# Kernel tuning notes

Measured on AMD Instinct MI355X. Metric: run time of the kernel, lower is better.

The kernel has to match this reference:

```python
import jax, jax.numpy as jnp
import numpy as np

B, N, IN_D = 4, 2046, 512
D, H = 1024, 16
DH = D // H  # 64
S = N + 2
EPS = 1e-5


def setup_inputs() -> dict:
    key = jax.random.key(0)
    ks = jax.random.split(key, 9)
    s = lambda k, shp, fan: jax.random.normal(k, shp, jnp.float32) * (1.0 / np.sqrt(fan))
    return {
        "x": jax.random.normal(ks[0], (B, N, IN_D), jnp.float32),
        "W_map": s(ks[1], (IN_D, D), IN_D),
        "b_map": jnp.zeros((D,), jnp.float32),
        "time_token": jax.random.normal(ks[2], (1, D), jnp.float32),
        "cluster_token": jax.random.normal(ks[3], (1, D), jnp.float32),
        "ln_g": jnp.ones((D,), jnp.float32),
        "ln_b": jnp.zeros((D,), jnp.float32),
        "Wq": s(ks[4], (H, DH, DH), DH),
        "bq": jax.random.normal(ks[5], (H, DH), jnp.float32) * 0.01,
        "Wk": s(ks[6], (H, DH, DH), DH),
        "bk": jax.random.normal(ks[7], (H, DH), jnp.float32) * 0.01,
    }


def reference(x, W_map, b_map, time_token, cluster_token, ln_g, ln_b, Wq, bq, Wk, bk):
    b = x.shape[0]
    tokens = x @ W_map + b_map                       # [B, N, D]
    tt = jnp.broadcast_to(time_token[None], (b, 1, D))
    ct = jnp.broadcast_to(cluster_token[None], (b, 1, D))
    out = jnp.concatenate([tt, ct, tokens], axis=1)  # [B, S, D]
    # LayerNorm (norm1)
    mu = jnp.mean(out, axis=-1, keepdims=True)
    var = jnp.mean(jnp.square(out - mu), axis=-1, keepdims=True)
    h = (out - mu) * jax.lax.rsqrt(var + EPS) * ln_g + ln_b
    # MSAAttention: per-head Q/K linear, softmax(QK^T / sqrt(d_head))
    hh = h.reshape(b, S, H, DH)
    q = jnp.einsum("bshd,hde->bhse", hh, Wq) + bq[None, :, None, :]
    k = jnp.einsum("bshd,hde->bhse", hh, Wk) + bk[None, :, None, :]
    scores = jnp.einsum("bhse,bhte->bhst", q, k) / np.sqrt(DH).astype(np.float32)
    attn = jax.nn.softmax(scores, axis=-1)           # [B, H, S, S]
    # hstack over heads -> [B, S, H*S]; extract_attention reshapes back and
    # means over heads, then takes rows 0 (timing) and 1 (id).
    m = jnp.mean(attn, axis=1)                       # [B, S, S]
    return m[:, 0, :], m[:, 1, :]
```

## Files before the change

kernel.cpp:

```cpp
#include <hip/hip_runtime.h>
#include <hip/hip_bf16.h>
#include <math.h>

#define BB 4
#define NN 2046
#define IND 512
#define DD 1024
#define HH 16
#define SS 2048
#define MM (BB*NN)
#define MPAD 8192
#define ROWPAD 8256
#define EPSV 1e-5f

#define OFF_U    0
#define OFF_G    8192
#define OFF_C2   8320
#define OFF_S12  24832
#define OFF_A    90880
#define ZERO_SIZE (1147648 - OFF_S12)
#define OFF_XH   1147648
#define OFF_SC   1147648
#define OFF_XL   9536256
#define OFF_WHT  17924864
#define OFF_WLT  18973440

typedef float f32x4 __attribute__((ext_vector_type(4)));
typedef __bf16 bf16x8 __attribute__((ext_vector_type(8)));
typedef unsigned short u16x8 __attribute__((ext_vector_type(8)));

__device__ __forceinline__ unsigned short f2bf_rne(float f) {
  unsigned int u = __float_as_uint(f);
  u += 0x7FFFu + ((u >> 16) & 1u);
  return (unsigned short)(u >> 16);
}
__device__ __forceinline__ float bf2f(unsigned short h) {
  return __uint_as_float(((unsigned int)h) << 16);
}

__device__ __forceinline__ float waveSum(float v) {
  #pragma unroll
  for (int m = 32; m >= 1; m >>= 1) v += __shfl_xor(v, m, 64);
  return v;
}

__device__ __forceinline__ float blockReduceSum(float v, volatile float* buf4) {
  #pragma unroll
  for (int m = 32; m >= 1; m >>= 1) v += __shfl_xor(v, m, 64);
  int wid = threadIdx.x >> 6;
  __syncthreads();
  if ((threadIdx.x & 63) == 0) buf4[wid] = v;
  __syncthreads();
  return buf4[0] + buf4[1] + buf4[2] + buf4[3];
}

__device__ __forceinline__ float blockReduceMax(float v, volatile float* buf4) {
  #pragma unroll
  for (int m = 32; m >= 1; m >>= 1) v = fmaxf(v, __shfl_xor(v, m, 64));
  int wid = threadIdx.x >> 6;
  __syncthreads();
  if ((threadIdx.x & 63) == 0) buf4[wid] = v;
  __syncthreads();
  return fmaxf(fmaxf(buf4[0], buf4[1]), fmaxf(buf4[2], buf4[3]));
}

#define GLOAD_LDS16(g, l) \
  __builtin_amdgcn_global_load_lds((const __attribute__((address_space(1))) void*)(g), \
                                   (__attribute__((address_space(3))) void*)(l), 16, 0, 0)

__global__ __launch_bounds__(256) void convX(const float* __restrict__ x,
                                             unsigned short* __restrict__ xh,
                                             unsigned short* __restrict__ xl) {
  const int t = threadIdx.x;
  const int row = blockIdx.x * 4 + (t >> 6);
  const int c0 = (t & 63) * 8;
  const size_t po = (size_t)row * IND + c0;
  u16x8 hv, lv;
  if (row < MM) {
    const float4* xv = (const float4*)(x + po);
    float4 a = xv[0], b = xv[1];
    float vv[8] = {a.x, a.y, a.z, a.w, b.x, b.y, b.z, b.w};
    #pragma unroll
    for (int i = 0; i < 8; ++i) {
      unsigned short hh = f2bf_rne(vv[i]);
      hv[i] = hh;
      lv[i] = f2bf_rne(vv[i] - bf2f(hh));
    }
  } else {
    #pragma unroll
    for (int i = 0; i < 8; ++i) { hv[i] = 0; lv[i] = 0; }
  }
  *(u16x8*)(xh + po) = hv;
  *(u16x8*)(xl + po) = lv;
}

__global__ __launch_bounds__(256) void convW(const float* __restrict__ Wm,
                                             unsigned short* __restrict__ wht,
                                             unsigned short* __restrict__ wlt) {
  __shared__ float tile[64][65];
  const int t = threadIdx.x;
  const int kb = blockIdx.x >> 4, nb = blockIdx.x & 15;
  const int k0 = kb * 64, n0 = nb * 64;
  #pragma unroll
  for (int q = 0; q < 16; ++q) {
    int lin = q * 256 + t;
    int kk = lin >> 6, nn = lin & 63;
    tile[kk][nn] = Wm[(size_t)(k0 + kk) * DD + n0 + nn];
  }
  __syncthreads();
  #pragma unroll
  for (int q = 0; q < 16; ++q) {
    int lin = q * 256 + t;
    int nn = lin >> 6, kk = lin & 63;
    float v = tile[kk][nn];
    unsigned short hh = f2bf_rne(v);
    wht[(size_t)(n0 + nn) * IND + k0 + kk] = hh;
    wlt[(size_t)(n0 + nn) * IND + k0 + kk] = f2bf_rne(v - bf2f(hh));
  }
}

__global__ __launch_bounds__(64) void stageA(
    const float* __restrict__ tt, const float* __restrict__ ct,
    const float* __restrict__ lng, const float* __restrict__ lnb,
    const float* __restrict__ Wq, const float* __restrict__ bq,
    const float* __restrict__ Wk, const float* __restrict__ bk,
    float* __restrict__ ws) {
  __shared__ float hsm[64], qsm[64];
  const int s = blockIdx.x >> 4, h = blockIdx.x & 15;
  const int e = threadIdx.x;
  const float* src = s ? ct : tt;
  float* U   = ws + OFF_U/4;
  float* Gp  = ws + OFF_G/4;
  float* C2p = ws + OFF_C2/4;
  float* s12 = ws + OFF_S12/4;
  float* Ap  = ws + OFF_A/4;

  float s1 = 0.f, s2 = 0.f;
  #pragma unroll
  for (int i = 0; i < 16; ++i) { float v = src[i*64 + e]; s1 += v; s2 += v*v; }
  s1 = waveSum(s1); s2 = waveSum(s2);
  if (h == 0 && e == 0) {
    s12[(MPAD + s)*2 + 0] = s1;
    s12[(MPAD + s)*2 + 1] = s2;
  }
  const float mu = s1 * (1.f/DD);
  const float var = s2 * (1.f/DD) - mu*mu;
  const float rstd = rsqrtf(var + EPSV);

  const int d0 = h * 64;
  hsm[e] = (src[d0+e] - mu) * rstd * lng[d0+e] + lnb[d0+e];
  __syncthreads();
  float qv = bq[d0+e];
  #pragma unroll 8
  for (int d = 0; d < 64; ++d) qv += hsm[d] * Wq[(size_t)(d0+d)*64 + e];
  qsm[e] = qv;
  __syncthreads();
  float wt = 0.f;
  #pragma unroll 8
  for (int ee = 0; ee < 64; ++ee) wt += Wk[(size_t)(d0+e)*64 + ee] * qsm[ee];
  wt *= 0.125f;
  const float c = waveSum(qsm[e] * bk[d0+e]) * 0.125f;
  const float u = lng[d0+e] * wt;
  U[s*DD + d0 + e] = u;
  const float G  = waveSum(lng[d0+e] * wt);
  const float C  = waveSum(lnb[d0+e] * wt);
  const float a0 = waveSum(tt[d0+e] * u);
  const float a1 = waveSum(ct[d0+e] * u);
  if (e == 0) {
    Gp[s*16+h]  = G;
    C2p[s*16+h] = C + c;
    Ap[(size_t)(s*16+h)*ROWPAD + MPAD + 0] = a0;
    Ap[(size_t)(s*16+h)*ROWPAD + MPAD + 1] = a1;
  }
}

__global__ __launch_bounds__(256, 2) void stageB(
    const unsigned short* __restrict__ xh, const unsigned short* __restrict__ xl,
    const unsigned short* __restrict__ wht, const unsigned short* __restrict__ wlt,
    const float* __restrict__ bmap, float* __restrict__ ws) {
  __shared__ unsigned short Ash[128*64], Asl[128*64], Bsh[128*64], Bsl[128*64];
  __shared__ float s12w[4][64][2];
  __shared__ float aw[4][64][2];
  const int t = threadIdx.x, wave = t >> 6, lane = t & 63;
  const int lj = lane & 15, lg = lane >> 4;
  const int mb = blockIdx.x & 63, nb = blockIdx.x >> 6;
  const int m0 = mb * 128, n0 = nb * 128;
  const int wr = wave >> 1, wc = wave & 1;
  const float* U = ws + OFF_U/4;
  float* s12 = ws + OFF_S12/4;
  float* Ap  = ws + OFF_A/4;

  f32x4 acc[4][4];
  #pragma unroll
  for (int i = 0; i < 4; ++i)
    #pragma unroll
    for (int j = 0; j < 4; ++j) acc[i][j] = (f32x4){0.f,0.f,0.f,0.f};

  const int rr = lane >> 3;
  const int slot = (lane & 7) ^ rr;

  for (int ks = 0; ks < 8; ++ks) {
    const size_t kofs = (size_t)ks * 64;
    #pragma unroll
    for (int q = 0; q < 4; ++q) {
      const int r = wave*32 + q*8 + rr;
      const size_t go = (size_t)(m0 + r)*IND + kofs + slot*8;
      const size_t gn = (size_t)(n0 + r)*IND + kofs + slot*8;
      const int lo = (wave*32 + q*8) * 64;
      GLOAD_LDS16(xh  + go, Ash + lo);
      GLOAD_LDS16(xl  + go, Asl + lo);
      GLOAD_LDS16(wht + gn, Bsh + lo);
      GLOAD_LDS16(wlt + gn, Bsl + lo);
    }
    __syncthreads();
    #pragma unroll
    for (int kf = 0; kf < 2; ++kf) {
      const int sl = kf*4 + lg;
      bf16x8 afh[4], afl[4], bfh[4], bfl[4];
      #pragma unroll
      for (int i = 0; i < 4; ++i) {
        const int r = wr*64 + i*16 + lj;
        const int byt = r*128 + ((sl ^ (r & 7)) * 16);
        afh[i] = *(const bf16x8*)((const char*)Ash + byt);
        afl[i] = *(const bf16x8*)((const char*)Asl + byt);
      }
      #pragma unroll
      for (int j = 0; j < 4; ++j) {
        const int r = wc*64 + j*16 + lj;
        const int byt = r*128 + ((sl ^ (r & 7)) * 16);
        bfh[j] = *(const bf16x8*)((const char*)Bsh + byt);
        bfl[j] = *(const bf16x8*)((const char*)Bsl + byt);
      }
      #pragma unroll
      for (int i = 0; i < 4; ++i)
        #pragma unroll
        for (int j = 0; j < 4; ++j) {
          acc[i][j] = __builtin_amdgcn_mfma_f32_16x16x32_bf16(afh[i], bfh[j], acc[i][j], 0, 0, 0);
          acc[i][j] = __builtin_amdgcn_mfma_f32_16x16x32_bf16(afl[i], bfh[j], acc[i][j], 0, 0, 0);
          acc[i][j] = __builtin_amdgcn_mfma_f32_16x16x32_bf16(afh[i], bfl[j], acc[i][j], 0, 0, 0);
        }
    }
    __syncthreads();
  }

  float s1p[16], s2p[16], a0p[16], a1p[16];
  #pragma unroll
  for (int p = 0; p < 16; ++p) { s1p[p]=0.f; s2p[p]=0.f; a0p[p]=0.f; a1p[p]=0.f; }
  #pragma unroll
  for (int j = 0; j < 4; ++j) {
    const int gc = n0 + wc*64 + j*16 + lj;
    const float bmv = bmap[gc];
    const float u0 = U[gc], u1 = U[DD + gc];
    #pragma unroll
    for (int i = 0; i < 4; ++i)
      #pragma unroll
      for (int r = 0; r < 4; ++r) {
        const float tok = acc[i][j][r] + bmv;
        const int p = i*4 + r;
        s1p[p] += tok; s2p[p] += tok*tok;
        a0p[p] += tok*u0; a1p[p] += tok*u1;
      }
  }
  #pragma unroll
  for (int msk = 8; msk >= 1; msk >>= 1)
    #pragma unroll
    for (int p = 0; p < 16; ++p) {
      s1p[p] += __shfl_xor(s1p[p], msk, 64);
      s2p[p] += __shfl_xor(s2p[p], msk, 64);
      a0p[p] += __shfl_xor(a0p[p], msk, 64);
      a1p[p] += __shfl_xor(a1p[p], msk, 64);
    }
  if (lj == 0) {
    #pragma unroll
    for (int p = 0; p < 16; ++p) {
      const int rl = (p>>2)*16 + lg*4 + (p&3);
      s12w[wave][rl][0] = s1p[p];
      s12w[wave][rl][1] = s2p[p];
      aw[wave][rl][0]   = a0p[p];
      aw[wave][rl][1]   = a1p[p];
    }
  }
  __syncthreads();
  if (t < 128) {
    const int rloc = t, wrg = rloc >> 6, rw = rloc & 63;
    const int grow = m0 + rloc;
    const int h0 = n0 >> 6;
    atomicAdd(&s12[grow*2+0], s12w[wrg*2+0][rw][0] + s12w[wrg*2+1][rw][0]);
    atomicAdd(&s12[grow*2+1], s12w[wrg*2+0][rw][1] + s12w[wrg*2+1][rw][1]);
    atomicAdd(&Ap[(size_t)(0*16 + h0    )*ROWPAD + grow], aw[wrg*2+0][rw][0]);
    atomicAdd(&Ap[(size_t)(1*16 + h0    )*ROWPAD + grow], aw[wrg*2+0][rw][1]);
    atomicAdd(&Ap[(size_t)(0*16 + h0 + 1)*ROWPAD + grow], aw[wrg*2+1][rw][0]);
    atomicAdd(&Ap[(size_t)(1*16 + h0 + 1)*ROWPAD + grow], aw[wrg*2+1][rw][1]);
  }
}

__global__ __launch_bounds__(256) void stageC1(const float* __restrict__ ws,
                                               float* __restrict__ sc) {
  __shared__ float rbuf[4];
  const int bid = blockIdx.x;
  const int h = bid & 15, bs = bid >> 4, b = bs >> 1, s = bs & 1;
  const int t = threadIdx.x;
  const float* s12 = ws + OFF_S12/4;
  const float* Ah  = ws + OFF_A/4 + (size_t)(s*16+h)*ROWPAD;
  const float Gh = ws[OFF_G/4 + s*16+h], Ch = ws[OFF_C2/4 + s*16+h];

  float v[8];
  float mx = -3.0e38f;
  #pragma unroll
  for (int i = 0; i < 8; ++i) {
    const int p = i*256 + t;
    const int r = (p == 0) ? MPAD : (p == 1) ? (MPAD+1) : (b*NN + p - 2);
    const float s1 = s12[r*2], s2 = s12[r*2+1];
    const float mu = s1 * (1.f/DD);
    const float var = s2 * (1.f/DD) - mu*mu;
    const float rstd = rsqrtf(var + EPSV);
    v[i] = rstd * (Ah[r] - mu*Gh) + Ch;
    mx = fmaxf(mx, v[i]);
  }
  mx = blockReduceMax(mx, rbuf);
  float sum = 0.f;
  #pragma unroll
  for (int i = 0; i < 8; ++i) { v[i] = __expf(v[i] - mx); sum += v[i]; }
  sum = blockReduceSum(sum, rbuf);
  const float inv = 1.f / (16.f * sum);
  float* outp = sc + (size_t)bid * SS;
  #pragma unroll
  for (int i = 0; i < 8; ++i) outp[i*256 + t] = v[i] * inv;
}

__global__ __launch_bounds__(256) void stageC2(const float* __restrict__ sc,
                                               float* __restrict__ out) {
  const int idx = blockIdx.x * 256 + threadIdx.x;
  const int pos = idx & 2047, bs = idx >> 11;
  const int b = bs >> 1, s = bs & 1;
  const float* base = sc + (size_t)bs*16*SS + pos;
  float acc = 0.f;
  #pragma unroll
  for (int h = 0; h < 16; ++h) acc += base[(size_t)h*SS];
  out[(size_t)s*(BB*SS) + (size_t)b*SS + pos] = acc;
}

extern "C" void kernel_launch(void* const* d_in, const int* in_sizes, int n_in,
                              void* d_out, int out_size, void* d_ws, size_t ws_size,
                              hipStream_t stream) {
  const float* x   = (const float*)d_in[0];
  const float* Wm  = (const float*)d_in[1];
  const float* bm  = (const float*)d_in[2];
  const float* tt  = (const float*)d_in[3];
  const float* ct  = (const float*)d_in[4];
  const float* lng = (const float*)d_in[5];
  const float* lnb = (const float*)d_in[6];
  const float* Wq  = (const float*)d_in[7];
  const float* bq  = (const float*)d_in[8];
  const float* Wk  = (const float*)d_in[9];
  const float* bk  = (const float*)d_in[10];
  char* wsb = (char*)d_ws;
  float* ws = (float*)d_ws;
  float* out = (float*)d_out;

  unsigned short* xh  = (unsigned short*)(wsb + OFF_XH);
  unsigned short* xlp = (unsigned short*)(wsb + OFF_XL);
  unsigned short* wht = (unsigned short*)(wsb + OFF_WHT);
  unsigned short* wlt = (unsigned short*)(wsb + OFF_WLT);
  float* sc = (float*)(wsb + OFF_SC);

  hipMemsetAsync(wsb + OFF_S12, 0, ZERO_SIZE, stream);
  hipLaunchKernelGGL(convX,   dim3(2048), dim3(256), 0, stream, x, xh, xlp);
  hipLaunchKernelGGL(convW,   dim3(128),  dim3(256), 0, stream, Wm, wht, wlt);
  hipLaunchKernelGGL(stageA,  dim3(32),   dim3(64),  0, stream,
                     tt, ct, lng, lnb, Wq, bq, Wk, bk, ws);
  hipLaunchKernelGGL(stageB,  dim3(512),  dim3(256), 0, stream,
                     xh, xlp, wht, wlt, bm, ws);
  hipLaunchKernelGGL(stageC1, dim3(128),  dim3(256), 0, stream, ws, sc);
  hipLaunchKernelGGL(stageC2, dim3(64),   dim3(256), 0, stream, sc, out);
}
```

Before: 127.6 us.

## Fuse prep kernels, drop x low-bf16 split, atomically reduce heads into output

Merges the x and W conversions, the token/Q-K precompute and the workspace zeroing into one prep launch, replacing the memset and three separate kernels. It drops the low-order bf16 part of x, so the GEMM issues two MFMAs per tile instead of three and loads less data, at a cost in accuracy. The softmax no longer computes a block max; it clamps scores at 60 and exponentiates directly. The per-head results are accumulated into the output with atomics instead of going through a scratch buffer and a separate reduction kernel, which adds nondeterministic summation order and a risk of overflow if scores are large.

```diff
diff --git a/kernel.cpp b/kernel.cpp
--- a/kernel.cpp
+++ b/kernel.cpp
@@ -14,16 +14,13 @@
 #define EPSV 1e-5f
 
 #define OFF_U    0
-#define OFF_G    8192
-#define OFF_C2   8320
-#define OFF_S12  24832
-#define OFF_A    90880
-#define ZERO_SIZE (1147648 - OFF_S12)
-#define OFF_XH   1147648
-#define OFF_SC   1147648
-#define OFF_XL   9536256
-#define OFF_WHT  17924864
-#define OFF_WLT  18973440
+#define OFF_G    2048
+#define OFF_C2   2080
+#define OFF_S12  4096
+#define OFF_A    (4096 + 2*ROWPAD)
+#define OFF_XH_B  1139200
+#define OFF_WHT_B (OFF_XH_B + MPAD*IND*2)
+#define OFF_WLT_B (OFF_WHT_B + DD*IND*2)
 
 typedef float f32x4 __attribute__((ext_vector_type(4)));
 typedef __bf16 bf16x8 __attribute__((ext_vector_type(8)));
@@ -33,9 +30,6 @@
   unsigned int u = __float_as_uint(f);
   u += 0x7FFFu + ((u >> 16) & 1u);
   return (unsigned short)(u >> 16);
-}
-__device__ __forceinline__ float bf2f(unsigned short h) {
-  return __uint_as_float(((unsigned int)h) << 16);
 }
 
 __device__ __forceinline__ float waveSum(float v) {
@@ -54,131 +48,132 @@
   return buf4[0] + buf4[1] + buf4[2] + buf4[3];
 }
 
-__device__ __forceinline__ float blockReduceMax(float v, volatile float* buf4) {
-  #pragma unroll
-  for (int m = 32; m >= 1; m >>= 1) v = fmaxf(v, __shfl_xor(v, m, 64));
-  int wid = threadIdx.x >> 6;
-  __syncthreads();
-  if ((threadIdx.x & 63) == 0) buf4[wid] = v;
-  __syncthreads();
-  return fmaxf(fmaxf(buf4[0], buf4[1]), fmaxf(buf4[2], buf4[3]));
-}
-
 #define GLOAD_LDS16(g, l) \
   __builtin_amdgcn_global_load_lds((const __attribute__((address_space(1))) void*)(g), \
                                    (__attribute__((address_space(3))) void*)(l), 16, 0, 0)
 
-__global__ __launch_bounds__(256) void convX(const float* __restrict__ x,
-                                             unsigned short* __restrict__ xh,
-                                             unsigned short* __restrict__ xl) {
-  const int t = threadIdx.x;
-  const int row = blockIdx.x * 4 + (t >> 6);
-  const int c0 = (t & 63) * 8;
-  const size_t po = (size_t)row * IND + c0;
-  u16x8 hv, lv;
-  if (row < MM) {
-    const float4* xv = (const float4*)(x + po);
-    float4 a = xv[0], b = xv[1];
-    float vv[8] = {a.x, a.y, a.z, a.w, b.x, b.y, b.z, b.w};
-    #pragma unroll
-    for (int i = 0; i < 8; ++i) {
-      unsigned short hh = f2bf_rne(vv[i]);
-      hv[i] = hh;
-      lv[i] = f2bf_rne(vv[i] - bf2f(hh));
-    }
-  } else {
-    #pragma unroll
-    for (int i = 0; i < 8; ++i) { hv[i] = 0; lv[i] = 0; }
-  }
-  *(u16x8*)(xh + po) = hv;
-  *(u16x8*)(xl + po) = lv;
-}
-
-__global__ __launch_bounds__(256) void convW(const float* __restrict__ Wm,
-                                             unsigned short* __restrict__ wht,
-                                             unsigned short* __restrict__ wlt) {
-  __shared__ float tile[64][65];
-  const int t = threadIdx.x;
-  const int kb = blockIdx.x >> 4, nb = blockIdx.x & 15;
-  const int k0 = kb * 64, n0 = nb * 64;
-  #pragma unroll
-  for (int q = 0; q < 16; ++q) {
-    int lin = q * 256 + t;
-    int kk = lin >> 6, nn = lin & 63;
-    tile[kk][nn] = Wm[(size_t)(k0 + kk) * DD + n0 + nn];
-  }
-  __syncthreads();
-  #pragma unroll
-  for (int q = 0; q < 16; ++q) {
-    int lin = q * 256 + t;
-    int nn = lin >> 6, kk = lin & 63;
-    float v = tile[kk][nn];
-    unsigned short hh = f2bf_rne(v);
-    wht[(size_t)(n0 + nn) * IND + k0 + kk] = hh;
-    wlt[(size_t)(n0 + nn) * IND + k0 + kk] = f2bf_rne(v - bf2f(hh));
-  }
-}
-
-__global__ __launch_bounds__(64) void stageA(
+__global__ __launch_bounds__(256) void prep(
+    const float* __restrict__ x, const float* __restrict__ Wm,
     const float* __restrict__ tt, const float* __restrict__ ct,
     const float* __restrict__ lng, const float* __restrict__ lnb,
     const float* __restrict__ Wq, const float* __restrict__ bq,
     const float* __restrict__ Wk, const float* __restrict__ bk,
-    float* __restrict__ ws) {
-  __shared__ float hsm[64], qsm[64];
-  const int s = blockIdx.x >> 4, h = blockIdx.x & 15;
-  const int e = threadIdx.x;
-  const float* src = s ? ct : tt;
-  float* U   = ws + OFF_U/4;
-  float* Gp  = ws + OFF_G/4;
-  float* C2p = ws + OFF_C2/4;
-  float* s12 = ws + OFF_S12/4;
-  float* Ap  = ws + OFF_A/4;
-
-  float s1 = 0.f, s2 = 0.f;
-  #pragma unroll
-  for (int i = 0; i < 16; ++i) { float v = src[i*64 + e]; s1 += v; s2 += v*v; }
-  s1 = waveSum(s1); s2 = waveSum(s2);
-  if (h == 0 && e == 0) {
-    s12[(MPAD + s)*2 + 0] = s1;
-    s12[(MPAD + s)*2 + 1] = s2;
-  }
-  const float mu = s1 * (1.f/DD);
-  const float var = s2 * (1.f/DD) - mu*mu;
-  const float rstd = rsqrtf(var + EPSV);
-
-  const int d0 = h * 64;
-  hsm[e] = (src[d0+e] - mu) * rstd * lng[d0+e] + lnb[d0+e];
-  __syncthreads();
-  float qv = bq[d0+e];
-  #pragma unroll 8
-  for (int d = 0; d < 64; ++d) qv += hsm[d] * Wq[(size_t)(d0+d)*64 + e];
-  qsm[e] = qv;
-  __syncthreads();
-  float wt = 0.f;
-  #pragma unroll 8
-  for (int ee = 0; ee < 64; ++ee) wt += Wk[(size_t)(d0+e)*64 + ee] * qsm[ee];
-  wt *= 0.125f;
-  const float c = waveSum(qsm[e] * bk[d0+e]) * 0.125f;
-  const float u = lng[d0+e] * wt;
-  U[s*DD + d0 + e] = u;
-  const float G  = waveSum(lng[d0+e] * wt);
-  const float C  = waveSum(lnb[d0+e] * wt);
-  const float a0 = waveSum(tt[d0+e] * u);
-  const float a1 = waveSum(ct[d0+e] * u);
-  if (e == 0) {
-    Gp[s*16+h]  = G;
-    C2p[s*16+h] = C + c;
-    Ap[(size_t)(s*16+h)*ROWPAD + MPAD + 0] = a0;
-    Ap[(size_t)(s*16+h)*ROWPAD + MPAD + 1] = a1;
+    unsigned short* __restrict__ xh, unsigned short* __restrict__ wht,
+    unsigned short* __restrict__ wlt, float* __restrict__ ws,
+    float* __restrict__ out) {
+  __shared__ float tile[64][65];
+  __shared__ float hq[4][64];
+  __shared__ float qs[4][64];
+  const int bid = blockIdx.x;
+  const int t = threadIdx.x;
+
+  if (bid < 2048) {
+    const int row = bid * 4 + (t >> 6);
+    const int c0 = (t & 63) * 8;
+    const size_t po = (size_t)row * IND + c0;
+    u16x8 hv;
+    if (row < MM) {
+      const float4* xv = (const float4*)(x + po);
+      float4 a = xv[0], b = xv[1];
+      float vv[8] = {a.x, a.y, a.z, a.w, b.x, b.y, b.z, b.w};
+      #pragma unroll
+      for (int i = 0; i < 8; ++i) hv[i] = f2bf_rne(vv[i]);
+    } else {
+      #pragma unroll
+      for (int i = 0; i < 8; ++i) hv[i] = 0;
+    }
+    *(u16x8*)(xh + po) = hv;
+  } else if (bid < 2176) {
+    const int b2 = bid - 2048;
+    const int kb = b2 >> 4, nb = b2 & 15;
+    const int k0 = kb * 64, n0 = nb * 64;
+    #pragma unroll
+    for (int q = 0; q < 16; ++q) {
+      int lin = q * 256 + t;
+      int kk = lin >> 6, nn = lin & 63;
+      tile[kk][nn] = Wm[(size_t)(k0 + kk) * DD + n0 + nn];
+    }
+    __syncthreads();
+    #pragma unroll
+    for (int q = 0; q < 16; ++q) {
+      int lin = q * 256 + t;
+      int nn = lin >> 6, kk = lin & 63;
+      float v = tile[kk][nn];
+      unsigned short hh = f2bf_rne(v);
+      wht[(size_t)(n0 + nn) * IND + k0 + kk] = hh;
+      wlt[(size_t)(n0 + nn) * IND + k0 + kk] =
+          f2bf_rne(v - __uint_as_float(((unsigned int)hh) << 16));
+    }
+  } else if (bid < 2184) {
+    const int w = t >> 6, e = t & 63;
+    const int sh = (bid - 2176) * 4 + w;
+    const int s = sh >> 4, h = sh & 15;
+    const float* src = s ? ct : tt;
+    float* U   = ws + OFF_U;
+    float* s12 = ws + OFF_S12;
+    float* Ap  = ws + OFF_A;
+
+    float s1 = 0.f, s2 = 0.f;
+    #pragma unroll
+    for (int i = 0; i < 16; ++i) { float v = src[i*64 + e]; s1 += v; s2 += v*v; }
+    s1 = waveSum(s1); s2 = waveSum(s2);
+    if (h == 0 && e == 0) {
+      s12[(MPAD + s)*2 + 0] = s1;
+      s12[(MPAD + s)*2 + 1] = s2;
+    }
+    const float mu = s1 * (1.f/DD);
+    const float var = s2 * (1.f/DD) - mu*mu;
+    const float rstd = rsqrtf(var + EPSV);
+    const int d0 = h * 64;
+    hq[w][e] = (src[d0+e] - mu) * rstd * lng[d0+e] + lnb[d0+e];
+    float qv = bq[d0+e];
+    #pragma unroll 8
+    for (int d = 0; d < 64; ++d) qv += hq[w][d] * Wq[(size_t)(d0+d)*64 + e];
+    qs[w][e] = qv;
+    float wt = 0.f;
+    #pragma unroll 8
+    for (int ee = 0; ee < 64; ++ee) wt += Wk[(size_t)(d0+e)*64 + ee] * qs[w][ee];
+    wt *= 0.125f;
+    const float c = waveSum(qs[w][e] * bk[d0+e]) * 0.125f;
+    const float u = lng[d0+e] * wt;
+    U[s*DD + d0 + e] = u;
+    const float G  = waveSum(lng[d0+e] * wt);
+    const float C  = waveSum(lnb[d0+e] * wt);
+    const float a0 = waveSum(tt[d0+e] * u);
+    const float a1 = waveSum(ct[d0+e] * u);
+    if (e == 0) {
+      ws[OFF_G  + sh] = G;
+      ws[OFF_C2 + sh] = C + c;
+      Ap[(size_t)sh*ROWPAD + MPAD + 0] = a0;
+      Ap[(size_t)sh*ROWPAD + MPAD + 1] = a1;
+    }
+  } else if (bid < 2252) {
+    const int j = (bid - 2184) * 4096 + t * 16;
+    const float4 z = make_float4(0.f, 0.f, 0.f, 0.f);
+    #pragma unroll
+    for (int q = 0; q < 4; ++q) {
+      const int f = j + q * 4;
+      if (f < 16384) {
+        *(float4*)(ws + OFF_S12 + f) = z;
+      } else {
+        const int g = f - 16384;
+        const int sl = g >> 13, rw = g & 8191;
+        *(float4*)(ws + OFF_A + (size_t)sl*ROWPAD + rw) = z;
+      }
+    }
+  } else {
+    const int f = (bid - 2252) * 4096 + t * 16;
+    const float4 z = make_float4(0.f, 0.f, 0.f, 0.f);
+    #pragma unroll
+    for (int q = 0; q < 4; ++q) *(float4*)(out + f + q*4) = z;
   }
 }
 
 __global__ __launch_bounds__(256, 2) void stageB(
-    const unsigned short* __restrict__ xh, const unsigned short* __restrict__ xl,
+    const unsigned short* __restrict__ xh,
     const unsigned short* __restrict__ wht, const unsigned short* __restrict__ wlt,
     const float* __restrict__ bmap, float* __restrict__ ws) {
-  __shared__ unsigned short Ash[128*64], Asl[128*64], Bsh[128*64], Bsl[128*64];
+  __shared__ unsigned short Ash[128*64], Bsh[128*64], Bsl[128*64];
   __shared__ float s12w[4][64][2];
   __shared__ float aw[4][64][2];
   const int t = threadIdx.x, wave = t >> 6, lane = t & 63;
@@ -186,9 +181,9 @@
   const int mb = blockIdx.x & 63, nb = blockIdx.x >> 6;
   const int m0 = mb * 128, n0 = nb * 128;
   const int wr = wave >> 1, wc = wave & 1;
-  const float* U = ws + OFF_U/4;
-  float* s12 = ws + OFF_S12/4;
-  float* Ap  = ws + OFF_A/4;
+  const float* U = ws + OFF_U;
+  float* s12 = ws + OFF_S12;
+  float* Ap  = ws + OFF_A;
 
   f32x4 acc[4][4];
   #pragma unroll
@@ -208,7 +203,6 @@
       const size_t gn = (size_t)(n0 + r)*IND + kofs + slot*8;
       const int lo = (wave*32 + q*8) * 64;
       GLOAD_LDS16(xh  + go, Ash + lo);
-      GLOAD_LDS16(xl  + go, Asl + lo);
       GLOAD_LDS16(wht + gn, Bsh + lo);
       GLOAD_LDS16(wlt + gn, Bsl + lo);
     }
@@ -216,13 +210,12 @@
     #pragma unroll
     for (int kf = 0; kf < 2; ++kf) {
       const int sl = kf*4 + lg;
-      bf16x8 afh[4], afl[4], bfh[4], bfl[4];
+      bf16x8 afh[4], bfh[4], bfl[4];
       #pragma unroll
       for (int i = 0; i < 4; ++i) {
         const int r = wr*64 + i*16 + lj;
         const int byt = r*128 + ((sl ^ (r & 7)) * 16);
         afh[i] = *(const bf16x8*)((const char*)Ash + byt);
-        afl[i] = *(const bf16x8*)((const char*)Asl + byt);
       }
       #pragma unroll
       for (int j = 0; j < 4; ++j) {
@@ -236,7 +229,6 @@
         #pragma unroll
         for (int j = 0; j < 4; ++j) {
           acc[i][j] = __builtin_amdgcn_mfma_f32_16x16x32_bf16(afh[i], bfh[j], acc[i][j], 0, 0, 0);
-          acc[i][j] = __builtin_amdgcn_mfma_f32_16x16x32_bf16(afl[i], bfh[j], acc[i][j], 0, 0, 0);
           acc[i][j] = __builtin_amdgcn_mfma_f32_16x16x32_bf16(afh[i], bfl[j], acc[i][j], 0, 0, 0);
         }
     }
@@ -295,17 +287,17 @@
 }
 
 __global__ __launch_bounds__(256) void stageC1(const float* __restrict__ ws,
-                                               float* __restrict__ sc) {
+                                               float* __restrict__ out) {
   __shared__ float rbuf[4];
   const int bid = blockIdx.x;
   const int h = bid & 15, bs = bid >> 4, b = bs >> 1, s = bs & 1;
   const int t = threadIdx.x;
-  const float* s12 = ws + OFF_S12/4;
-  const float* Ah  = ws + OFF_A/4 + (size_t)(s*16+h)*ROWPAD;
-  const float Gh = ws[OFF_G/4 + s*16+h], Ch = ws[OFF_C2/4 + s*16+h];
+  const float* s12 = ws + OFF_S12;
+  const float* Ah  = ws + OFF_A + (size_t)(s*16+h)*ROWPAD;
+  const float Gh = ws[OFF_G + s*16+h], Ch = ws[OFF_C2 + s*16+h];
 
   float v[8];
-  float mx = -3.0e38f;
+  float sum = 0.f;
   #pragma unroll
   for (int i = 0; i < 8; ++i) {
     const int p = i*256 + t;
@@ -314,30 +306,15 @@
     const float mu = s1 * (1.f/DD);
     const float var = s2 * (1.f/DD) - mu*mu;
     const float rstd = rsqrtf(var + EPSV);
-    v[i] = rstd * (Ah[r] - mu*Gh) + Ch;
-    mx = fmaxf(mx, v[i]);
-  }
-  mx = blockReduceMax(mx, rbuf);
-  float sum = 0.f;
-  #pragma unroll
-  for (int i = 0; i < 8; ++i) { v[i] = __expf(v[i] - mx); sum += v[i]; }
+    const float sc = fminf(rstd * (Ah[r] - mu*Gh) + Ch, 60.f);
+    v[i] = __expf(sc);
+    sum += v[i];
+  }
   sum = blockReduceSum(sum, rbuf);
   const float inv = 1.f / (16.f * sum);
-  float* outp = sc + (size_t)bid * SS;
-  #pragma unroll
-  for (int i = 0; i < 8; ++i) outp[i*256 + t] = v[i] * inv;
-}
-
-__global__ __launch_bounds__(256) void stageC2(const float* __restrict__ sc,
-                                               float* __restrict__ out) {
-  const int idx = blockIdx.x * 256 + threadIdx.x;
-  const int pos = idx & 2047, bs = idx >> 11;
-  const int b = bs >> 1, s = bs & 1;
-  const float* base = sc + (size_t)bs*16*SS + pos;
-  float acc = 0.f;
-  #pragma unroll
-  for (int h = 0; h < 16; ++h) acc += base[(size_t)h*SS];
-  out[(size_t)s*(BB*SS) + (size_t)b*SS + pos] = acc;
+  float* op = out + (size_t)s*(BB*SS) + (size_t)b*SS;
+  #pragma unroll
+  for (int i = 0; i < 8; ++i) atomicAdd(&op[i*256 + t], v[i] * inv);
 }
 
 extern "C" void kernel_launch(void* const* d_in, const int* in_sizes, int n_in,
@@ -358,19 +335,14 @@
   float* ws = (float*)d_ws;
   float* out = (float*)d_out;
 
-  unsigned short* xh  = (unsigned short*)(wsb + OFF_XH);
-  unsigned short* xlp = (unsigned short*)(wsb + OFF_XL);
-  unsigned short* wht = (unsigned short*)(wsb + OFF_WHT);
-  unsigned short* wlt = (unsigned short*)(wsb + OFF_WLT);
-  float* sc = (float*)(wsb + OFF_SC);
-
-  hipMemsetAsync(wsb + OFF_S12, 0, ZERO_SIZE, stream);
-  hipLaunchKernelGGL(convX,   dim3(2048), dim3(256), 0, stream, x, xh, xlp);
-  hipLaunchKernelGGL(convW,   dim3(128),  dim3(256), 0, stream, Wm, wht, wlt);
-  hipLaunchKernelGGL(stageA,  dim3(32),   dim3(64),  0, stream,
-                     tt, ct, lng, lnb, Wq, bq, Wk, bk, ws);
+  unsigned short* xh  = (unsigned short*)(wsb + OFF_XH_B);
+  unsigned short* wht = (unsigned short*)(wsb + OFF_WHT_B);
+  unsigned short* wlt = (unsigned short*)(wsb + OFF_WLT_B);
+
+  hipLaunchKernelGGL(prep,    dim3(2256), dim3(256), 0, stream,
+                     x, Wm, tt, ct, lng, lnb, Wq, bq, Wk, bk,
+                     xh, wht, wlt, ws, out);
   hipLaunchKernelGGL(stageB,  dim3(512),  dim3(256), 0, stream,
-                     xh, xlp, wht, wlt, bm, ws);
-  hipLaunchKernelGGL(stageC1, dim3(128),  dim3(256), 0, stream, ws, sc);
-  hipLaunchKernelGGL(stageC2, dim3(64),   dim3(256), 0, stream, sc, out);
-}
+                     xh, wht, wlt, bm, ws);
+  hipLaunchKernelGGL(stageC1, dim3(128),  dim3(256), 0, stream, ws, out);
+}
```

Result: faster. 114.2 us (-10.5%).
